# Kernel optimization log

Hardware: AMD Instinct MI355X
Metric: run time of the kernel (lower is better)

The kernel has to match this reference:

```python
import jax, jax.numpy as jnp
import numpy as np

N, E = 50000, 300000
IN_DIM, CODE_DIM = 1024, 768
HID, HEADS, DH = 256, 4, 64
NUM_REL = 5
CODE_WEIGHT = 1.0


def setup_inputs() -> dict:
    key = jax.random.key(0)
    ks = jax.random.split(key, 24)
    p = lambda k, shape: jax.random.normal(k, shape, dtype=jnp.float32) * 0.05
    return {
        "x": jax.random.normal(ks[0], (N, IN_DIM), dtype=jnp.float32),
        "edge_index": jax.random.randint(ks[1], (2, E), 0, N, dtype=jnp.int64),
        "edge_type": jax.random.randint(ks[2], (E,), 0, NUM_REL, dtype=jnp.int64),
        "edge_weight": jax.random.uniform(ks[3], (E,), dtype=jnp.float32),
        "rel_emb": p(ks[4], (NUM_REL, HID)),
        "W_in": p(ks[5], (HID, IN_DIM)),
        "b_in": jnp.zeros((HID,), jnp.float32),
        "W1": p(ks[6], (HEADS * DH, HID)),
        "a1_src": p(ks[7], (HEADS, DH)),
        "a1_dst": p(ks[8], (HEADS, DH)),
        "b1": jnp.zeros((HEADS * DH,), jnp.float32),
        "W2": p(ks[9], (HEADS * DH, HID)),
        "a2_src": p(ks[10], (HEADS, DH)),
        "a2_dst": p(ks[11], (HEADS, DH)),
        "b2": jnp.zeros((HEADS * DH,), jnp.float32),
        "ln1_g": jnp.ones((HID,), jnp.float32),
        "ln1_b": jnp.zeros((HID,), jnp.float32),
        "ln2_g": jnp.ones((HID,), jnp.float32),
        "ln2_b": jnp.zeros((HID,), jnp.float32),
        "W_out": p(ks[12], (1, HID)),
        "b_out": jnp.zeros((1,), jnp.float32),
    }


def _layer_norm(x, g, b, eps=1e-5):
    m = x.mean(-1, keepdims=True)
    v = ((x - m) ** 2).mean(-1, keepdims=True)
    return (x - m) * jax.lax.rsqrt(v + eps) * g + b


def _gat_conv(h, s_all, d_all, W, a_src, a_dst, bias):
    # PyG GATConv (concat=True, negative_slope=0.2), self-loops already in s_all/d_all
    xh = (h @ W.T).reshape(N, HEADS, DH)                      # [N,H,DH]
    al_s = (xh * a_src).sum(-1)                                # [N,H]
    al_d = (xh * a_dst).sum(-1)                                # [N,H]
    e = jax.nn.leaky_relu(al_s[s_all] + al_d[d_all], 0.2)      # [E+N,H]
    mx = jax.ops.segment_max(e, d_all, num_segments=N)         # segment softmax over dst
    ex = jnp.exp(e - mx[d_all])
    den = jax.ops.segment_sum(ex, d_all, num_segments=N)
    alpha = ex / (den[d_all] + 1e-16)
    out = jax.ops.segment_sum(xh[s_all] * alpha[:, :, None], d_all, num_segments=N)
    return out.reshape(N, HEADS * DH) + bias


def reference(x, edge_index, edge_type, edge_weight, rel_emb, W_in, b_in,
              W1, a1_src, a1_dst, b1, W2, a2_src, a2_dst, b2,
              ln1_g, ln1_b, ln2_g, ln2_b, W_out, b_out):
    # split (code_at_front=True), standardize numeric, l2-normalize code
    x_code = x[:, :CODE_DIM]
    x_num = x[:, CODE_DIM:]
    m = x_num.mean(0, keepdims=True)
    s = jnp.maximum(x_num.std(0, ddof=1, keepdims=True), 1e-6)
    x_num = (x_num - m) / s
    nrm = jnp.maximum(jnp.linalg.norm(x_code, axis=1, keepdims=True), 1e-12)
    x_code = x_code / nrm
    xin = jnp.concatenate([x_num, CODE_WEIGHT * x_code], axis=-1)

    h = jax.nn.relu(xin @ W_in.T + b_in)                       # [N,HID]

    src, dst = edge_index[0], edge_index[1]
    rel = rel_emb[edge_type] * edge_weight[:, None]            # [E,HID]
    msg = h[src] + rel
    h = h.at[dst].add(msg)                                     # index_add

    loop = jnp.arange(N, dtype=src.dtype)                      # GATConv add_self_loops
    s_all = jnp.concatenate([src, loop])
    d_all = jnp.concatenate([dst, loop])

    h1 = _gat_conv(h, s_all, d_all, W1, a1_src, a1_dst, b1)
    h = _layer_norm(h1 + h, ln1_g, ln1_b)
    h2 = _gat_conv(h, s_all, d_all, W2, a2_src, a2_dst, b2)
    h = _layer_norm(h2 + h, ln2_g, ln2_b)
    return (h @ W_out.T + b_out).squeeze(-1)                   # [N]
```

## Files before the change

kernel.cpp:

```cpp
#include <hip/hip_runtime.h>
#include <math.h>

constexpr int NN   = 50000;
constexpr int EE   = 300000;
constexpr int IND  = 1024;
constexpr int CODE = 768;
constexpr int HID  = 256;

typedef __bf16 bf16_t;
typedef bf16_t bf16x8 __attribute__((ext_vector_type(8)));
typedef float  f32x4  __attribute__((ext_vector_type(4)));

__device__ __forceinline__ f32x4 mfma16(bf16x8 a, bf16x8 b, f32x4 c) {
    return __builtin_amdgcn_mfma_f32_16x16x32_bf16(a, b, c, 0, 0, 0);
}

#define GLOAD_LDS16(gp, lp) __builtin_amdgcn_global_load_lds(                         \
    (__attribute__((address_space(1))) void*)(gp),                                    \
    (__attribute__((address_space(3))) void*)(lp), 16, 0, 0)

__device__ __forceinline__ void cvt_split(f32x4 u0, f32x4 u1, bf16x8& hi, bf16x8& lo) {
    #pragma unroll
    for (int i = 0; i < 4; i++) {
        bf16_t h0 = (bf16_t)u0[i];
        hi[i]     = h0;
        lo[i]     = (bf16_t)(u0[i] - (float)h0);
        bf16_t h1 = (bf16_t)u1[i];
        hi[4 + i] = h1;
        lo[4 + i] = (bf16_t)(u1[i] - (float)h1);
    }
}

__global__ void colstats_kernel(const float* __restrict__ x, float* __restrict__ sums) {
    int col = threadIdx.x;
    float s = 0.f, s2 = 0.f;
    for (int row = blockIdx.x; row < NN; row += gridDim.x) {
        float v = x[(size_t)row * IND + CODE + col];
        s += v; s2 += v * v;
    }
    atomicAdd(&sums[col], s);
    atomicAdd(&sums[256 + col], s2);
}

__global__ void finalize_stats_kernel(const float* __restrict__ sums, float* __restrict__ mi) {
    int c = threadIdx.x;
    float mean = sums[c] / (float)NN;
    float var  = (sums[256 + c] - (float)NN * mean * mean) / (float)(NN - 1);
    float sd   = sqrtf(fmaxf(var, 0.f));
    sd = fmaxf(sd, 1e-6f);
    mi[c]       = mean;
    mi[256 + c] = 1.f / sd;
}

__global__ void prep_w_kernel(const float* __restrict__ W, const float* __restrict__ stats,
                              const float* __restrict__ b_in, bf16_t* __restrict__ Wh,
                              bf16_t* __restrict__ Wl, float* __restrict__ cb)
{
    int c = blockIdx.x, t = threadIdx.x;
    const float* wr = W + (size_t)c * IND;
    bf16_t* wh = Wh + (size_t)c * IND;
    bf16_t* wl = Wl + (size_t)c * IND;
    for (int k = t; k < 768; k += 256) {
        float v = wr[256 + k];
        bf16_t h = (bf16_t)v;
        wh[k] = h; wl[k] = (bf16_t)(v - (float)h);
    }
    {
        float v = wr[t] * stats[256 + t];
        bf16_t h = (bf16_t)v;
        wh[768 + t] = h; wl[768 + t] = (bf16_t)(v - (float)h);
    }
    float p = wr[t] * stats[256 + t] * stats[t];
    #pragma unroll
    for (int off = 32; off; off >>= 1) p += __shfl_xor(p, off);
    __shared__ float ps[4];
    if ((t & 63) == 0) ps[t >> 6] = p;
    __syncthreads();
    if (t == 0) cb[c] = b_in[c] - (ps[0] + ps[1] + ps[2] + ps[3]);
}

__global__ void prep_ws_kernel(const float* __restrict__ W, bf16_t* __restrict__ Wh,
                               bf16_t* __restrict__ Wl)
{
    int c = blockIdx.x, t = threadIdx.x;
    float v = W[(size_t)c * 256 + t];
    bf16_t h = (bf16_t)v;
    Wh[(size_t)c * 256 + t] = h;
    Wl[(size_t)c * 256 + t] = (bf16_t)(v - (float)h);
}


__device__ __forceinline__ void stage_a(const float* __restrict__ src, int ldk,
                                        int rowbase, int maxrow, int k0,
                                        float* ldsbuf, int tid) {
    int w = tid >> 6, l = tid & 63;
    int lr = l >> 3, lc = l & 7;
    int g  = lc ^ lr;
    #pragma unroll
    for (int i = 0; i < 4; i++) {
        int rloc = i * 32 + w * 8;
        float* dst = ldsbuf + rloc * 32;
        int row = rowbase + rloc + lr;
        if (row > maxrow) row = maxrow;
        const float* gp = src + (size_t)row * ldk + k0 + g * 4;
        GLOAD_LDS16(gp, dst);
    }
}

__device__ __forceinline__ void stage_b(const bf16_t* __restrict__ src, int n0, int ldk,
                                        int k0, bf16_t* buf, int tid) {
    int w = tid >> 6, l = tid & 63;
    #pragma unroll
    for (int i = 0; i < 2; i++) {
        int gbase = w * 128 + i * 64;
        bf16_t* dst = buf + gbase * 8;
        int g = gbase + l;
        int col = g >> 2, p = g & 3;
        int gs = p ^ ((col >> 1) & 3);
        const bf16_t* gp = src + (size_t)(n0 + col) * ldk + k0 + gs * 8;
        GLOAD_LDS16(gp, dst);
    }
}

template<int MODE, int K, int FATTN>
__global__ __launch_bounds__(256) void gemm_mfma_kernel(
    const float* __restrict__ A, const bf16_t* __restrict__ Bh,
    const bf16_t* __restrict__ Bl, const float* __restrict__ cb,
    const float* __restrict__ a_src, const float* __restrict__ a_dst,
    float* __restrict__ out, float* __restrict__ al_s, float* __restrict__ al_d)
{
    __shared__ float  As[2][128 * 32];
    __shared__ bf16_t Bhs[2][128 * 32];
    __shared__ bf16_t Bls[2][128 * 32];
    constexpr int NT = K / 32;

    int tid  = threadIdx.x;
    int lane = tid & 63;
    int w    = tid >> 6;
    int wr   = w >> 1, wc = w & 1;
    int r0   = blockIdx.x * 128, n0 = blockIdx.y * 128;

    f32x4 acc[4][4];
    #pragma unroll
    for (int i = 0; i < 4; i++)
        #pragma unroll
        for (int j = 0; j < 4; j++) acc[i][j] = (f32x4)0.f;

    float ss[4] = {0.f, 0.f, 0.f, 0.f};

    int kc = lane >> 4, fr = lane & 15;

    stage_a(A, K, r0, NN - 1, 0, As[0], tid);
    stage_b(Bh, n0, K, 0, Bhs[0], tid);
    stage_b(Bl, n0, K, 0, Bls[0], tid);
    __syncthreads();

    for (int t = 0; t < NT; ++t) {
        int buf = t & 1;
        if (t + 1 < NT) {
            stage_a(A, K, r0, NN - 1, (t + 1) * 32, As[buf ^ 1], tid);
            stage_b(Bh, n0, K, (t + 1) * 32, Bhs[buf ^ 1], tid);
            stage_b(Bl, n0, K, (t + 1) * 32, Bls[buf ^ 1], tid);
        }
        if (MODE == 1 && t == 24) {
            #pragma unroll
            for (int mf = 0; mf < 4; mf++) {
                float s2 = ss[mf];
                s2 += __shfl_xor(s2, 16);
                s2 += __shfl_xor(s2, 32);
                #pragma unroll
                for (int j = 0; j < 4; j++) {
                    float sv = __shfl(s2, kc * 4 + j);
                    float iv = 1.f / fmaxf(sqrtf(sv), 1e-12f);
                    #pragma unroll
                    for (int nf = 0; nf < 4; nf++) acc[mf][nf][j] *= iv;
                }
            }
        }
        const float*  Ab = As[buf];
        const bf16_t* Hb = Bhs[buf];
        const bf16_t* Lb = Bls[buf];
        bf16x8 ahi[4], alo[4];
        #pragma unroll
        for (int mf = 0; mf < 4; mf++) {
            int r  = wr * 64 + mf * 16 + fr;
            int rb = r * 32, r7 = r & 7;
            f32x4 u0 = *(const f32x4*)&Ab[rb + (((2 * kc + 0) ^ r7) << 2)];
            f32x4 u1 = *(const f32x4*)&Ab[rb + (((2 * kc + 1) ^ r7) << 2)];
            if (MODE == 1 && t < 24) {
                #pragma unroll
                for (int q = 0; q < 4; q++) ss[mf] += u0[q] * u0[q] + u1[q] * u1[q];
            }
            cvt_split(u0, u1, ahi[mf], alo[mf]);
        }
        #pragma unroll
        for (int nf = 0; nf < 4; nf++) {
            int c  = wc * 64 + nf * 16 + fr;
            int pr = kc ^ ((c >> 1) & 3);
            bf16x8 bhi = *(const bf16x8*)&Hb[c * 32 + pr * 8];
            bf16x8 blo = *(const bf16x8*)&Lb[c * 32 + pr * 8];
            #pragma unroll
            for (int mf = 0; mf < 4; mf++) {
                acc[mf][nf] = mfma16(ahi[mf], bhi, acc[mf][nf]);
                acc[mf][nf] = mfma16(alo[mf], bhi, acc[mf][nf]);
                acc[mf][nf] = mfma16(ahi[mf], blo, acc[mf][nf]);
            }
        }
        __syncthreads();
    }

    int head = blockIdx.y * 2 + wc;
    float asv[4], adv[4];
    if (FATTN) {
        #pragma unroll
        for (int nf = 0; nf < 4; nf++) {
            asv[nf] = a_src[head * 64 + nf * 16 + fr];
            adv[nf] = a_dst[head * 64 + nf * 16 + fr];
        }
    }
    #pragma unroll
    for (int mf = 0; mf < 4; mf++) {
        #pragma unroll
        for (int j = 0; j < 4; j++) {
            int row = r0 + wr * 64 + mf * 16 + kc * 4 + j;
            bool ok = row < NN;
            float s = 0.f, d = 0.f;
            #pragma unroll
            for (int nf = 0; nf < 4; nf++) {
                int col = n0 + wc * 64 + nf * 16 + fr;
                float v = acc[mf][nf][j];
                if (MODE == 1) v = fmaxf(v + cb[col], 0.f);
                if (ok) out[(size_t)row * HID + col] = v;
                if (FATTN) { s += v * asv[nf]; d += v * adv[nf]; }
            }
            if (FATTN) {
                #pragma unroll
                for (int off = 1; off < 16; off <<= 1) {
                    s += __shfl_xor(s, off);
                    d += __shfl_xor(d, off);
                }
                if (ok && fr == 0) {
                    al_s[row * 4 + head] = s;
                    al_d[row * 4 + head] = d;
                }
            }
        }
    }
}

__global__ void deg_kernel(const int* __restrict__ ei, int* __restrict__ deg) {
    int e = blockIdx.x * 256 + threadIdx.x;
    if (e < EE) atomicAdd(&deg[ei[EE + e]], 1);
}

constexpr int SCB = 1024;
constexpr int SCN = (NN + SCB - 1) / SCB;

__global__ void scan_pass1(const int* __restrict__ deg, int* __restrict__ bsum) {
    int b = blockIdx.x, t = threadIdx.x;
    int base = b * SCB + t * 4;
    int s = 0;
    #pragma unroll
    for (int i = 0; i < 4; i++) { int idx = base + i; if (idx < NN) s += deg[idx]; }
    #pragma unroll
    for (int off = 32; off; off >>= 1) s += __shfl_xor(s, off);
    __shared__ int ps[4];
    if ((t & 63) == 0) ps[t >> 6] = s;
    __syncthreads();
    if (t == 0) bsum[b] = ps[0] + ps[1] + ps[2] + ps[3];
}

__global__ void scan_pass2(int* __restrict__ bsum) {
    int t = threadIdx.x;
    int orig = (t < SCN) ? bsum[t] : 0;
    int v = orig;
    for (int off = 1; off < 64; off <<= 1) {
        int u = __shfl_up(v, off);
        if (t >= off) v += u;
    }
    if (t < SCN) bsum[t] = v - orig;
}

__global__ void scan_pass3(const int* __restrict__ deg, const int* __restrict__ boffs,
                           int* __restrict__ row_ptr, int* __restrict__ cursor) {
    int b = blockIdx.x, t = threadIdx.x;
    int base = b * SCB + t * 4;
    int d[4]; int tot = 0;
    #pragma unroll
    for (int i = 0; i < 4; i++) { int idx = base + i; d[i] = (idx < NN) ? deg[idx] : 0; tot += d[i]; }
    int v = tot;
    for (int off = 1; off < 64; off <<= 1) {
        int u = __shfl_up(v, off);
        if ((t & 63) >= off) v += u;
    }
    __shared__ int wsum[4];
    if ((t & 63) == 63) wsum[t >> 6] = v;
    __syncthreads();
    int woff = 0;
    for (int j = 0; j < (t >> 6); j++) woff += wsum[j];
    int run = boffs[b] + woff + v - tot;
    #pragma unroll
    for (int i = 0; i < 4; i++) {
        int idx = base + i;
        if (idx < NN) {
            cursor[idx] = run;
            run += d[i];
            row_ptr[idx + 1] = run;
        }
    }
    if (b == 0 && t == 0) row_ptr[0] = 0;
}

__global__ void fill_kernel(const int* __restrict__ ei, const int* __restrict__ etype,
                            const float* __restrict__ ew, int* __restrict__ cursor,
                            int* __restrict__ csr_src, int* __restrict__ csr_t,
                            float* __restrict__ csr_w) {
    int e = blockIdx.x * 256 + threadIdx.x;
    if (e >= EE) return;
    int dst = ei[EE + e];
    int pos = atomicAdd(&cursor[dst], 1);
    csr_src[pos] = ei[e];
    csr_t[pos]   = etype[e];
    csr_w[pos]   = ew[e];
}

__global__ void relagg_kernel(const float* __restrict__ h, const int* __restrict__ row_ptr,
                              const int* __restrict__ csr_src, const int* __restrict__ csr_t,
                              const float* __restrict__ csr_w,
                              const float* __restrict__ rel_emb, float* __restrict__ out)
{
    int lane = threadIdx.x & 63, wid = threadIdx.x >> 6;
    int node = blockIdx.x * 4 + wid;
    if (node >= NN) return;
    const float* hr = h + (size_t)node * HID;
    float acc[4];
    #pragma unroll
    for (int c = 0; c < 4; c++) acc[c] = hr[c * 64 + lane];
    float wsum[5] = {0.f, 0.f, 0.f, 0.f, 0.f};
    int beg = row_ptr[node], end = row_ptr[node + 1];
    int k = beg;
    for (; k + 4 <= end; k += 4) {
        int s[4], tt[4]; float ww[4];
        #pragma unroll
        for (int j = 0; j < 4; j++) {
            s[j]  = csr_src[k + j];
            tt[j] = csr_t[k + j];
            ww[j] = csr_w[k + j];
        }
        float xv[4][4];
        #pragma unroll
        for (int j = 0; j < 4; j++) {
            const float* hs = h + (size_t)s[j] * HID;
            #pragma unroll
            for (int c = 0; c < 4; c++) xv[j][c] = hs[c * 64 + lane];
        }
        #pragma unroll
        for (int j = 0; j < 4; j++) {
            #pragma unroll
            for (int c = 0; c < 4; c++) acc[c] += xv[j][c];
            #pragma unroll
            for (int r = 0; r < 5; r++) wsum[r] += (tt[j] == r) ? ww[j] : 0.f;
        }
    }
    for (; k < end; k++) {
        int src = csr_src[k]; int t = csr_t[k]; float w = csr_w[k];
        const float* hs = h + (size_t)src * HID;
        #pragma unroll
        for (int c = 0; c < 4; c++) acc[c] += hs[c * 64 + lane];
        #pragma unroll
        for (int r = 0; r < 5; r++) wsum[r] += (t == r) ? w : 0.f;
    }
    #pragma unroll
    for (int r = 0; r < 5; r++)
        #pragma unroll
        for (int c = 0; c < 4; c++) acc[c] += wsum[r] * rel_emb[r * HID + c * 64 + lane];
    float* o = out + (size_t)node * HID;
    #pragma unroll
    for (int c = 0; c < 4; c++) o[c * 64 + lane] = acc[c];
}

template<int FINAL>
__global__ void gat_kernel(const float* __restrict__ xh, const float* __restrict__ al_s,
                           const float* __restrict__ al_d, const int* __restrict__ row_ptr,
                           const int* __restrict__ csr_src, const float* __restrict__ h_res,
                           const float* __restrict__ bias, const float* __restrict__ ln_g,
                           const float* __restrict__ ln_b, float* __restrict__ out,
                           const float* __restrict__ W_out, const float* __restrict__ b_out,
                           float* __restrict__ final_out)
{
    int lane = threadIdx.x & 63, wid = threadIdx.x >> 6;
    int node = blockIdx.x * 4 + wid;
    if (node >= NN) return;

    float4 aldv = *(const float4*)&al_d[node * 4];
    float ald[4] = {aldv.x, aldv.y, aldv.z, aldv.w};
    float m[4], den[4], acc[4];

    {
        float4 alsv = *(const float4*)&al_s[node * 4];
        float als[4] = {alsv.x, alsv.y, alsv.z, alsv.w};
        const float* xs = xh + (size_t)node * HID;
        #pragma unroll
        for (int hh = 0; hh < 4; hh++) {
            float e = als[hh] + ald[hh];
            e = (e >= 0.f) ? e : 0.2f * e;
            m[hh] = e; den[hh] = 1.f;
            acc[hh] = xs[hh * 64 + lane];
        }
    }

    int beg = row_ptr[node], end = row_ptr[node + 1];
    int k = beg;
    for (; k + 4 <= end; k += 4) {
        int s[4];
        #pragma unroll
        for (int j = 0; j < 4; j++) s[j] = csr_src[k + j];
        float4 av[4];
        #pragma unroll
        for (int j = 0; j < 4; j++) av[j] = *(const float4*)&al_s[s[j] * 4];
        float xv[4][4];
        #pragma unroll
        for (int j = 0; j < 4; j++) {
            const float* xs = xh + (size_t)s[j] * HID;
            #pragma unroll
            for (int hh = 0; hh < 4; hh++) xv[j][hh] = xs[hh * 64 + lane];
        }
        #pragma unroll
        for (int j = 0; j < 4; j++) {
            float als[4] = {av[j].x, av[j].y, av[j].z, av[j].w};
            #pragma unroll
            for (int hh = 0; hh < 4; hh++) {
                float e = als[hh] + ald[hh];
                e = (e >= 0.f) ? e : 0.2f * e;
                float mn  = fmaxf(m[hh], e);
                float f   = __expf(m[hh] - mn);
                float wgt = __expf(e - mn);
                m[hh]   = mn;
                den[hh] = den[hh] * f + wgt;
                acc[hh] = acc[hh] * f + wgt * xv[j][hh];
            }
        }
    }
    for (; k < end; k++) {
        int src = csr_src[k];
        float4 alsv = *(const float4*)&al_s[src * 4];
        float als[4] = {alsv.x, alsv.y, alsv.z, alsv.w};
        const float* xs = xh + (size_t)src * HID;
        #pragma unroll
        for (int hh = 0; hh < 4; hh++) {
            float e = als[hh] + ald[hh];
            e = (e >= 0.f) ? e : 0.2f * e;
            float mn  = fmaxf(m[hh], e);
            float f   = __expf(m[hh] - mn);
            float wgt = __expf(e - mn);
            m[hh]   = mn;
            den[hh] = den[hh] * f + wgt;
            acc[hh] = acc[hh] * f + wgt * xs[hh * 64 + lane];
        }
    }

    float z[4];
    #pragma unroll
    for (int hh = 0; hh < 4; hh++) {
        int c = hh * 64 + lane;
        z[hh] = acc[hh] / (den[hh] + 1e-16f) + bias[c] + h_res[(size_t)node * HID + c];
    }
    float s = z[0] + z[1] + z[2] + z[3];
    #pragma unroll
    for (int off = 32; off; off >>= 1) s += __shfl_xor(s, off);
    float mean = s * (1.f / 256.f);
    float vp = 0.f;
    #pragma unroll
    for (int hh = 0; hh < 4; hh++) { float d2 = z[hh] - mean; vp += d2 * d2; }
    #pragma unroll
    for (int off = 32; off; off >>= 1) vp += __shfl_xor(vp, off);
    float rstd = rsqrtf(vp * (1.f / 256.f) + 1e-5f);

    if (FINAL) {
        float dot = 0.f;
        #pragma unroll
        for (int hh = 0; hh < 4; hh++) {
            int c = hh * 64 + lane;
            float v = (z[hh] - mean) * rstd * ln_g[c] + ln_b[c];
            dot += v * W_out[c];
        }
        #pragma unroll
        for (int off = 32; off; off >>= 1) dot += __shfl_xor(dot, off);
        if (lane == 0) final_out[node] = dot + b_out[0];
    } else {
        #pragma unroll
        for (int hh = 0; hh < 4; hh++) {
            int c = hh * 64 + lane;
            out[(size_t)node * HID + c] = (z[hh] - mean) * rstd * ln_g[c] + ln_b[c];
        }
    }
}

extern "C" void kernel_launch(void* const* d_in, const int* in_sizes, int n_in,
                              void* d_out, int out_size, void* d_ws, size_t ws_size,
                              hipStream_t stream) {
    const float* x       = (const float*)d_in[0];
    const int*   ei      = (const int*)d_in[1];
    const int*   etype   = (const int*)d_in[2];
    const float* ew      = (const float*)d_in[3];
    const float* rel_emb = (const float*)d_in[4];
    const float* W_in    = (const float*)d_in[5];
    const float* b_in    = (const float*)d_in[6];
    const float* W1      = (const float*)d_in[7];
    const float* a1s     = (const float*)d_in[8];
    const float* a1d     = (const float*)d_in[9];
    const float* b1      = (const float*)d_in[10];
    const float* W2      = (const float*)d_in[11];
    const float* a2s     = (const float*)d_in[12];
    const float* a2d     = (const float*)d_in[13];
    const float* b2      = (const float*)d_in[14];
    const float* ln1g    = (const float*)d_in[15];
    const float* ln1b    = (const float*)d_in[16];
    const float* ln2g    = (const float*)d_in[17];
    const float* ln2b    = (const float*)d_in[18];
    const float* W_out   = (const float*)d_in[19];
    const float* b_out   = (const float*)d_in[20];
    float* out = (float*)d_out;

    char* ws = (char*)d_ws;
    auto alloc = [&](size_t bytes) {
        void* p = (void*)ws;
        ws += (bytes + 255) & ~(size_t)255;
        return p;
    };
    float*  bufA     = (float*)alloc((size_t)NN * HID * 4);
    float*  bufB     = (float*)alloc((size_t)NN * HID * 4);
    float*  bufC     = (float*)alloc((size_t)NN * HID * 4);
    bf16_t* wmh      = (bf16_t*)alloc((size_t)HID * IND * 2);
    bf16_t* wml      = (bf16_t*)alloc((size_t)HID * IND * 2);
    bf16_t* w1h      = (bf16_t*)alloc((size_t)HID * HID * 2);
    bf16_t* w1l      = (bf16_t*)alloc((size_t)HID * HID * 2);
    bf16_t* w2h      = (bf16_t*)alloc((size_t)HID * HID * 2);
    bf16_t* w2l      = (bf16_t*)alloc((size_t)HID * HID * 2);
    float*  cbv      = (float*)alloc(256 * 4);
    float*  stats_s  = (float*)alloc(512 * 4);
    float*  stats_mi = (float*)alloc(512 * 4);
    float*  al_s     = (float*)alloc((size_t)NN * 4 * 4);
    float*  al_d     = (float*)alloc((size_t)NN * 4 * 4);
    int*    deg      = (int*)alloc((size_t)NN * 4);
    int*    row_ptr  = (int*)alloc((size_t)(NN + 1) * 4);
    int*    cursor   = (int*)alloc((size_t)NN * 4);
    int*    csr_src  = (int*)alloc((size_t)EE * 4);
    int*    csr_t    = (int*)alloc((size_t)EE * 4);
    float*  csr_w    = (float*)alloc((size_t)EE * 4);
    int*    bsum     = (int*)alloc(64 * 4);

    hipMemsetAsync(stats_s, 0, 512 * 4, stream);
    hipMemsetAsync(deg, 0, (size_t)NN * 4, stream);

    colstats_kernel<<<1024, 256, 0, stream>>>(x, stats_s);
    finalize_stats_kernel<<<1, 256, 0, stream>>>(stats_s, stats_mi);
    prep_w_kernel<<<256, 256, 0, stream>>>(W_in, stats_mi, b_in, wmh, wml, cbv);
    prep_ws_kernel<<<256, 256, 0, stream>>>(W1, w1h, w1l);
    prep_ws_kernel<<<256, 256, 0, stream>>>(W2, w2h, w2l);

    deg_kernel<<<(EE + 255) / 256, 256, 0, stream>>>(ei, deg);
    scan_pass1<<<SCN, 256, 0, stream>>>(deg, bsum);
    scan_pass2<<<1, 64, 0, stream>>>(bsum);
    scan_pass3<<<SCN, 256, 0, stream>>>(deg, bsum, row_ptr, cursor);
    fill_kernel<<<(EE + 255) / 256, 256, 0, stream>>>(ei, etype, ew, cursor,
                                                      csr_src, csr_t, csr_w);

    dim3 g1((NN + 127) / 128, 2);

    gemm_mfma_kernel<1, 1024, 0><<<g1, 256, 0, stream>>>(
        x, wmh, wml, cbv, nullptr, nullptr, bufA, nullptr, nullptr);

    int nodeBlocks = (NN + 3) / 4;

    relagg_kernel<<<nodeBlocks, 256, 0, stream>>>(bufA, row_ptr, csr_src, csr_t, csr_w,
                                                  rel_emb, bufB);

    gemm_mfma_kernel<0, 256, 1><<<g1, 256, 0, stream>>>(
        bufB, w1h, w1l, nullptr, a1s, a1d, bufC, al_s, al_d);
    gat_kernel<0><<<nodeBlocks, 256, 0, stream>>>(bufC, al_s, al_d, row_ptr, csr_src,
                                                  bufB, b1, ln1g, ln1b, bufA,
                                                  nullptr, nullptr, nullptr);

    gemm_mfma_kernel<0, 256, 1><<<g1, 256, 0, stream>>>(
        bufA, w2h, w2l, nullptr, a2s, a2d, bufC, al_s, al_d);
    gat_kernel<1><<<nodeBlocks, 256, 0, stream>>>(bufC, al_s, al_d, row_ptr, csr_src,
                                                  bufA, b2, ln2g, ln2b, nullptr,
                                                  W_out, b_out, out);
}
```

Before: 501.5 us.

## Store GAT projections as bf16 and precompute code row norms separately

The GAT projection GEMMs now write their output only as a bf16 copy, and the gat kernels gather neighbor features from that bf16 buffer instead of fp32. This halves the bytes of the random gathers in the edge aggregation. Separately, the L2 norm of each code row moves into a new rownorm kernel, which removes the per-tile sum-of-squares work from the input GEMM. The costs are an extra pass over 768 columns of x and lower precision in the aggregated features.

After: 495.8 us. Within noise of the previous version (-1.2%).

```diff
diff --git a/kernel.cpp b/kernel.cpp
--- a/kernel.cpp
+++ b/kernel.cpp
@@ -50,6 +50,23 @@
     sd = fmaxf(sd, 1e-6f);
     mi[c]       = mean;
     mi[256 + c] = 1.f / sd;
+}
+
+__global__ void rownorm_kernel(const float* __restrict__ x, float* __restrict__ invnorm) {
+    int lane = threadIdx.x & 63;
+    int wid  = threadIdx.x >> 6;
+    int row  = blockIdx.x * 4 + wid;
+    if (row >= NN) return;
+    const float4* x4 = (const float4*)(x + (size_t)row * IND);
+    float s = 0.f;
+    #pragma unroll
+    for (int i = 0; i < 3; i++) {
+        float4 v = x4[lane + i * 64];
+        s += v.x * v.x + v.y * v.y + v.z * v.z + v.w * v.w;
+    }
+    #pragma unroll
+    for (int off = 32; off; off >>= 1) s += __shfl_xor(s, off);
+    if (lane == 0) invnorm[row] = 1.f / fmaxf(sqrtf(s), 1e-12f);
 }
 
 __global__ void prep_w_kernel(const float* __restrict__ W, const float* __restrict__ stats,
@@ -126,12 +143,14 @@
 __global__ __launch_bounds__(256) void gemm_mfma_kernel(
     const float* __restrict__ A, const bf16_t* __restrict__ Bh,
     const bf16_t* __restrict__ Bl, const float* __restrict__ cb,
-    const float* __restrict__ a_src, const float* __restrict__ a_dst,
-    float* __restrict__ out, float* __restrict__ al_s, float* __restrict__ al_d)
+    const float* __restrict__ invnorm, const float* __restrict__ a_src,
+    const float* __restrict__ a_dst, float* __restrict__ out,
+    bf16_t* __restrict__ xhb, float* __restrict__ al_s, float* __restrict__ al_d)
 {
     __shared__ float  As[2][128 * 32];
     __shared__ bf16_t Bhs[2][128 * 32];
     __shared__ bf16_t Bls[2][128 * 32];
+    __shared__ float inv_s[128];
     constexpr int NT = K / 32;
 
     int tid  = threadIdx.x;
@@ -140,13 +159,16 @@
     int wr   = w >> 1, wc = w & 1;
     int r0   = blockIdx.x * 128, n0 = blockIdx.y * 128;
 
+    if (MODE == 1 && tid < 128) {
+        int r = r0 + tid;
+        inv_s[tid] = (r < NN) ? invnorm[r] : 1.f;
+    }
+
     f32x4 acc[4][4];
     #pragma unroll
     for (int i = 0; i < 4; i++)
         #pragma unroll
         for (int j = 0; j < 4; j++) acc[i][j] = (f32x4)0.f;
-
-    float ss[4] = {0.f, 0.f, 0.f, 0.f};
 
     int kc = lane >> 4, fr = lane & 15;
 
@@ -165,16 +187,11 @@
         if (MODE == 1 && t == 24) {
             #pragma unroll
             for (int mf = 0; mf < 4; mf++) {
-                float s2 = ss[mf];
-                s2 += __shfl_xor(s2, 16);
-                s2 += __shfl_xor(s2, 32);
+                f32x4 iv = *(const f32x4*)&inv_s[wr * 64 + mf * 16 + kc * 4];
                 #pragma unroll
-                for (int j = 0; j < 4; j++) {
-                    float sv = __shfl(s2, kc * 4 + j);
-                    float iv = 1.f / fmaxf(sqrtf(sv), 1e-12f);
+                for (int nf = 0; nf < 4; nf++)
                     #pragma unroll
-                    for (int nf = 0; nf < 4; nf++) acc[mf][nf][j] *= iv;
-                }
+                    for (int j = 0; j < 4; j++) acc[mf][nf][j] *= iv[j];
             }
         }
         const float*  Ab = As[buf];
@@ -187,10 +204,6 @@
             int rb = r * 32, r7 = r & 7;
             f32x4 u0 = *(const f32x4*)&Ab[rb + (((2 * kc + 0) ^ r7) << 2)];
             f32x4 u1 = *(const f32x4*)&Ab[rb + (((2 * kc + 1) ^ r7) << 2)];
-            if (MODE == 1 && t < 24) {
-                #pragma unroll
-                for (int q = 0; q < 4; q++) ss[mf] += u0[q] * u0[q] + u1[q] * u1[q];
-            }
             cvt_split(u0, u1, ahi[mf], alo[mf]);
         }
         #pragma unroll
@@ -229,9 +242,14 @@
             for (int nf = 0; nf < 4; nf++) {
                 int col = n0 + wc * 64 + nf * 16 + fr;
                 float v = acc[mf][nf][j];
-                if (MODE == 1) v = fmaxf(v + cb[col], 0.f);
-                if (ok) out[(size_t)row * HID + col] = v;
-                if (FATTN) { s += v * asv[nf]; d += v * adv[nf]; }
+                if (MODE == 1) {
+                    v = fmaxf(v + cb[col], 0.f);
+                    if (ok) out[(size_t)row * HID + col] = v;
+                }
+                if (FATTN) {
+                    s += v * asv[nf]; d += v * adv[nf];
+                    if (ok) xhb[(size_t)row * HID + col] = (bf16_t)v;
+                }
             }
             if (FATTN) {
                 #pragma unroll
@@ -380,7 +398,7 @@
 }
 
 template<int FINAL>
-__global__ void gat_kernel(const float* __restrict__ xh, const float* __restrict__ al_s,
+__global__ void gat_kernel(const bf16_t* __restrict__ xhb, const float* __restrict__ al_s,
                            const float* __restrict__ al_d, const int* __restrict__ row_ptr,
                            const int* __restrict__ csr_src, const float* __restrict__ h_res,
                            const float* __restrict__ bias, const float* __restrict__ ln_g,
@@ -399,13 +417,13 @@
     {
         float4 alsv = *(const float4*)&al_s[node * 4];
         float als[4] = {alsv.x, alsv.y, alsv.z, alsv.w};
-        const float* xs = xh + (size_t)node * HID;
+        const bf16_t* xs = xhb + (size_t)node * HID;
         #pragma unroll
         for (int hh = 0; hh < 4; hh++) {
             float e = als[hh] + ald[hh];
             e = (e >= 0.f) ? e : 0.2f * e;
             m[hh] = e; den[hh] = 1.f;
-            acc[hh] = xs[hh * 64 + lane];
+            acc[hh] = (float)xs[hh * 64 + lane];
         }
     }
 
@@ -421,9 +439,9 @@
         float xv[4][4];
         #pragma unroll
         for (int j = 0; j < 4; j++) {
-            const float* xs = xh + (size_t)s[j] * HID;
-            #pragma unroll
-            for (int hh = 0; hh < 4; hh++) xv[j][hh] = xs[hh * 64 + lane];
+            const bf16_t* xs = xhb + (size_t)s[j] * HID;
+            #pragma unroll
+            for (int hh = 0; hh < 4; hh++) xv[j][hh] = (float)xs[hh * 64 + lane];
         }
         #pragma unroll
         for (int j = 0; j < 4; j++) {
@@ -445,7 +463,7 @@
         int src = csr_src[k];
         float4 alsv = *(const float4*)&al_s[src * 4];
         float als[4] = {alsv.x, alsv.y, alsv.z, alsv.w};
-        const float* xs = xh + (size_t)src * HID;
+        const bf16_t* xs = xhb + (size_t)src * HID;
         #pragma unroll
         for (int hh = 0; hh < 4; hh++) {
             float e = als[hh] + ald[hh];
@@ -455,7 +473,7 @@
             float wgt = __expf(e - mn);
             m[hh]   = mn;
             den[hh] = den[hh] * f + wgt;
-            acc[hh] = acc[hh] * f + wgt * xs[hh * 64 + lane];
+            acc[hh] = acc[hh] * f + wgt * (float)xs[hh * 64 + lane];
         }
     }
 
@@ -530,7 +548,7 @@
     };
     float*  bufA     = (float*)alloc((size_t)NN * HID * 4);
     float*  bufB     = (float*)alloc((size_t)NN * HID * 4);
-    float*  bufC     = (float*)alloc((size_t)NN * HID * 4);
+    bf16_t* xhb      = (bf16_t*)alloc((size_t)NN * HID * 2);
     bf16_t* wmh      = (bf16_t*)alloc((size_t)HID * IND * 2);
     bf16_t* wml      = (bf16_t*)alloc((size_t)HID * IND * 2);
     bf16_t* w1h      = (bf16_t*)alloc((size_t)HID * HID * 2);
@@ -540,6 +558,7 @@
     float*  cbv      = (float*)alloc(256 * 4);
     float*  stats_s  = (float*)alloc(512 * 4);
     float*  stats_mi = (float*)alloc(512 * 4);
+    float*  invnorm  = (float*)alloc((size_t)NN * 4);
     float*  al_s     = (float*)alloc((size_t)NN * 4 * 4);
     float*  al_d     = (float*)alloc((size_t)NN * 4 * 4);
     int*    deg      = (int*)alloc((size_t)NN * 4);
@@ -555,6 +574,7 @@
 
     colstats_kernel<<<1024, 256, 0, stream>>>(x, stats_s);
     finalize_stats_kernel<<<1, 256, 0, stream>>>(stats_s, stats_mi);
+    rownorm_kernel<<<(NN + 3) / 4, 256, 0, stream>>>(x, invnorm);
     prep_w_kernel<<<256, 256, 0, stream>>>(W_in, stats_mi, b_in, wmh, wml, cbv);
     prep_ws_kernel<<<256, 256, 0, stream>>>(W1, w1h, w1l);
     prep_ws_kernel<<<256, 256, 0, stream>>>(W2, w2h, w2l);
@@ -569,7 +589,7 @@
     dim3 g1((NN + 127) / 128, 2);
 
     gemm_mfma_kernel<1, 1024, 0><<<g1, 256, 0, stream>>>(
-        x, wmh, wml, cbv, nullptr, nullptr, bufA, nullptr, nullptr);
+        x, wmh, wml, cbv, invnorm, nullptr, nullptr, bufA, nullptr, nullptr, nullptr);
 
     int nodeBlocks = (NN + 3) / 4;
 
@@ -577,14 +597,14 @@
                                                   rel_emb, bufB);
 
     gemm_mfma_kernel<0, 256, 1><<<g1, 256, 0, stream>>>(
-        bufB, w1h, w1l, nullptr, a1s, a1d, bufC, al_s, al_d);
-    gat_kernel<0><<<nodeBlocks, 256, 0, stream>>>(bufC, al_s, al_d, row_ptr, csr_src,
+        bufB, w1h, w1l, nullptr, nullptr, a1s, a1d, nullptr, xhb, al_s, al_d);
+    gat_kernel<0><<<nodeBlocks, 256, 0, stream>>>(xhb, al_s, al_d, row_ptr, csr_src,
                                                   bufB, b1, ln1g, ln1b, bufA,
                                                   nullptr, nullptr, nullptr);
 
     gemm_mfma_kernel<0, 256, 1><<<g1, 256, 0, stream>>>(
-        bufA, w2h, w2l, nullptr, a2s, a2d, bufC, al_s, al_d);
-    gat_kernel<1><<<nodeBlocks, 256, 0, stream>>>(bufC, al_s, al_d, row_ptr, csr_src,
+        bufA, w2h, w2l, nullptr, nullptr, a2s, a2d, nullptr, xhb, al_s, al_d);
+    gat_kernel<1><<<nodeBlocks, 256, 0, stream>>>(xhb, al_s, al_d, row_ptr, csr_src,
                                                   bufA, b2, ln2g, ln2b, nullptr,
                                                   W_out, b_out, out);
 }
```
